# Kernel tuning notes

Hardware: AMD Instinct MI355X
Metric: run time of the kernel (lower is better)

## Reference

```python
import jax, jax.numpy as jnp
import numpy as np

N, E = 20000, 640000
D_IN, D_H, D_OUT = 128, 64, 32


def _lin_w(key, out_d, in_d):
    return jax.random.normal(key, (out_d, in_d), jnp.float32) / np.sqrt(in_d)


def setup_inputs() -> dict:
    key = jax.random.key(0)
    ks = jax.random.split(key, 16)
    x = jax.random.normal(ks[0], (N, D_IN), jnp.float32)
    edge_index = jax.random.randint(ks[1], (2, E), 0, N, jnp.int64)
    inp = {"x": x, "edge_index": edge_index}
    # SAGEConv weights: lin_l (aggregated neighbors, with bias), lin_r (root, no bias)
    inp["Wl1"] = _lin_w(ks[2], D_H, D_IN); inp["bl1"] = jnp.zeros((D_H,), jnp.float32)
    inp["Wr1"] = _lin_w(ks[3], D_H, D_IN)
    inp["Wl2"] = _lin_w(ks[4], D_H, D_H); inp["bl2"] = jnp.zeros((D_H,), jnp.float32)
    inp["Wr2"] = _lin_w(ks[5], D_H, D_H)
    inp["Wl3"] = _lin_w(ks[6], D_OUT, D_H); inp["bl3"] = jnp.zeros((D_OUT,), jnp.float32)
    inp["Wr3"] = _lin_w(ks[7], D_OUT, D_H)
    # Conv2d kernels (OIHW), all 3x3 pad 1
    inp["Wc1"] = jax.random.normal(ks[8], (D_H, 1, 3, 3), jnp.float32) / 3.0
    inp["bc1"] = jnp.zeros((D_H,), jnp.float32)
    inp["Wc2"] = jax.random.normal(ks[9], (D_H, D_H, 3, 3), jnp.float32) / np.sqrt(9 * D_H)
    inp["bc2"] = jnp.zeros((D_H,), jnp.float32)
    inp["Wc3"] = jax.random.normal(ks[10], (1, D_H, 3, 3), jnp.float32) / np.sqrt(9 * D_H)
    inp["bc3"] = jnp.zeros((1,), jnp.float32)
    # linear2 (hidden -> hidden)
    inp["W2"] = _lin_w(ks[11], D_H, D_H); inp["b2"] = jnp.zeros((D_H,), jnp.float32)
    return inp


def _sage(x, src, dst, Wl, bl, Wr):
    # PyG SAGEConv (mean aggr): lin_l(mean_{j->i} x_j) + lin_r(x_i)
    msg = x[src]  # [E, d] gather
    agg = jax.ops.segment_sum(msg, dst, num_segments=N)
    deg = jax.ops.segment_sum(jnp.ones((src.shape[0], 1), x.dtype), dst, num_segments=N)
    agg = agg / jnp.maximum(deg, 1.0)
    return agg @ Wl.T + bl + x @ Wr.T


def _conv(x, w, b):
    y = jax.lax.conv_general_dilated(x, w, (1, 1), ((1, 1), (1, 1)),
                                     dimension_numbers=("NCHW", "OIHW", "NCHW"))
    return y + b[None, :, None, None]


def reference(x, edge_index, Wl1, bl1, Wr1, Wl2, bl2, Wr2, Wl3, bl3, Wr3,
              Wc1, bc1, Wc2, bc2, Wc3, bc3, W2, b2):
    src, dst = edge_index[0], edge_index[1]
    h = _sage(x, src, dst, Wl1, bl1, Wr1)
    h = _sage(h, src, dst, Wl2, bl2, Wr2)
    h = _sage(h, src, dst, Wl2, bl2, Wr2)  # sage2 reused, as in source
    out_1 = h
    h4 = h[None, None]                     # [1,1,N,D_H]
    out = _conv(h4, Wc1, bc1)              # [1,D_H,N,D_H]
    out = _conv(out, Wc2, bc2)             # dropout is identity at inference
    out = _conv(out, Wc3, bc3)             # [1,1,N,D_H]
    out = out[0, 0] + out_1
    out = out @ W2.T + b2
    h = _sage(out, src, dst, Wl2, bl2, Wr2)
    h = _sage(h, src, dst, Wl2, bl2, Wr2)
    h = _sage(h, src, dst, Wl3, bl3, Wr3)
    return h
```

## Files before the change

kernel.cpp:

```cpp
#include <hip/hip_runtime.h>

#define NN 20000
#define NE 640000
#define NBUK 79

__device__ __forceinline__ int probe_stride(const int* __restrict__ ei32) {
  int lane = threadIdx.x & 63;
  int v = ei32[2 * lane + 1];
  unsigned long long nz = __ballot(v != 0);
  return (nz == 0ull) ? 2 : 1;
}

__global__ __launch_bounds__(256) void k_histB(const int* __restrict__ ei,
                                               int* __restrict__ bins, int E) {
  __shared__ int lb[NBUK];
  int tid = threadIdx.x;
  int st = probe_stride(ei);
  for (int i = tid; i < NBUK; i += 256) lb[i] = 0;
  __syncthreads();
  int e0 = blockIdx.x * 4096;
#pragma unroll
  for (int t = 0; t < 16; ++t) {
    int e = e0 + t * 256 + tid;
    if (e < E) atomicAdd(&lb[ei[(size_t)(E + e) * st] >> 8], 1);
  }
  __syncthreads();
  for (int i = tid; i < NBUK; i += 256)
    if (lb[i]) atomicAdd(&bins[i], lb[i]);
}

__global__ __launch_bounds__(128) void k_scan79(const int* __restrict__ bins,
                                                int* __restrict__ bbase,
                                                int* __restrict__ bcur,
                                                int* __restrict__ rowptr,
                                                int E, int N) {
  __shared__ int lds[128];
  int tid = threadIdx.x;
  int mine = (tid < NBUK) ? bins[tid] : 0;
  lds[tid] = mine;
  __syncthreads();
  for (int off = 1; off < 128; off <<= 1) {
    int v = (tid >= off) ? lds[tid - off] : 0;
    __syncthreads();
    lds[tid] += v;
    __syncthreads();
  }
  int ex = lds[tid] - mine;
  if (tid <= NBUK) {
    bbase[tid] = ex;
    if (tid < NBUK) bcur[tid] = ex;
  }
  if (tid == 0) rowptr[N] = E;
}

__global__ __launch_bounds__(256) void k_part(const int* __restrict__ ei,
                                              int* __restrict__ bcur,
                                              unsigned long long* __restrict__ ebuf,
                                              int E) {
  __shared__ int lcnt[NBUK];
  __shared__ int lbase[NBUK];
  int tid = threadIdx.x;
  int st = probe_stride(ei);
  for (int i = tid; i < NBUK; i += 256) lcnt[i] = 0;
  __syncthreads();
  int e0 = blockIdx.x * 4096;
  int srcv[16], dstv[16], lrank[16], bk[16];
  int n = 0;
#pragma unroll
  for (int t = 0; t < 16; ++t) {
    int e = e0 + t * 256 + tid;
    if (e < E) {
      int s = ei[(size_t)e * st];
      int d = ei[(size_t)(E + e) * st];
      int b = d >> 8;
      srcv[n] = s; dstv[n] = d; bk[n] = b;
      lrank[n] = atomicAdd(&lcnt[b], 1);
      ++n;
    }
  }
  __syncthreads();
  for (int i = tid; i < NBUK; i += 256)
    lbase[i] = atomicAdd(&bcur[i], lcnt[i]);
  __syncthreads();
  for (int t = 0; t < n; ++t) {
    int pos = lbase[bk[t]] + lrank[t];
    ebuf[pos] = ((unsigned long long)(unsigned)dstv[t] << 32) | (unsigned)srcv[t];
  }
}

__global__ __launch_bounds__(256) void k_sortb(
    const unsigned long long* __restrict__ ebuf, const int* __restrict__ bbase,
    int* __restrict__ rowptr, float* __restrict__ invdeg,
    int* __restrict__ csr, int N) {
  __shared__ int lcnt[256];
  __shared__ int lcur[256];
  __shared__ int wsum[4];
  int b = blockIdx.x;
  int tid = threadIdx.x;
  int base = bbase[b], n = bbase[b + 1] - base;
  lcnt[tid] = 0;
  __syncthreads();
  for (int e = tid; e < n; e += 256) {
    int d = (int)(ebuf[base + e] >> 32);
    atomicAdd(&lcnt[d - (b << 8)], 1);
  }
  __syncthreads();
  int c = lcnt[tid];
  int lane = tid & 63, wid = tid >> 6;
  int s = c;
#pragma unroll
  for (int off = 1; off < 64; off <<= 1) {
    int v = __shfl_up(s, off, 64);
    if (lane >= off) s += v;
  }
  if (lane == 63) wsum[wid] = s;
  __syncthreads();
  int woff = 0;
  for (int w = 0; w < wid; ++w) woff += wsum[w];
  int pref = woff + s - c;
  int gnode = (b << 8) + tid;
  if (gnode < N) {
    rowptr[gnode] = base + pref;
    invdeg[gnode] = 1.0f / (float)(c < 1 ? 1 : c);
  }
  lcur[tid] = pref;
  __syncthreads();
  for (int e = tid; e < n; e += 256) {
    unsigned long long pk = ebuf[base + e];
    int d = (int)(pk >> 32);
    int pos = atomicAdd(&lcur[d - (b << 8)], 1);
    csr[base + pos] = (int)(unsigned)pk;
  }
}

__device__ __forceinline__ bool maskB(int var, int o2, int o1) {
  int s = o2 + o1;
  switch (var) {
    case 0: return (o2 >= 0) && (s >= 0);
    case 1: return s >= -1;
    case 3: return s <= 1;
    case 4: return (o2 <= 0) && (s <= 0);
    default: return true;
  }
}

__global__ __launch_bounds__(256) void k_setup2(
    const float* __restrict__ Wc1, const float* __restrict__ Wc2,
    const float* __restrict__ Wc3, const float* __restrict__ bc1,
    const float* __restrict__ bc2, const float* __restrict__ bc3,
    const float* __restrict__ Wl1, const float* __restrict__ Wr1,
    const float* __restrict__ Wl2, const float* __restrict__ Wr2,
    const float* __restrict__ Wl3, const float* __restrict__ Wr3,
    const float* __restrict__ W2, const float* __restrict__ b2,
    float* __restrict__ T729, float* __restrict__ beta5,
    float* __restrict__ Wf, float* __restrict__ bf,
    float* __restrict__ Wt1, float* __restrict__ Wt2,
    float* __restrict__ Wt3, float* __restrict__ W2t) {
  int b = blockIdx.x, tid = threadIdx.x;
  if (b == 0) {
    __shared__ float W3[576];
    __shared__ float S9s[5184];
    __shared__ float W1s[576];
    for (int e = tid; e < 576; e += 256) { W3[e] = Wc3[e]; W1s[e] = Wc1[e]; }
    __syncthreads();
    for (int bb = tid; bb < 576; bb += 256) {
      float acc[9];
#pragma unroll
      for (int a = 0; a < 9; ++a) acc[a] = 0.0f;
#pragma unroll 4
      for (int o = 0; o < 64; ++o) {
        float w2 = Wc2[o * 576 + bb];
#pragma unroll
        for (int a = 0; a < 9; ++a) acc[a] += W3[o * 9 + a] * w2;
      }
#pragma unroll
      for (int a = 0; a < 9; ++a) S9s[a * 576 + bb] = acc[a];
    }
    __syncthreads();
    for (int c = tid; c < 729; c += 256) {
      int kx0  = c % 3;
      int dl1e = (c / 3) % 3;
      int dl2e = (c / 9) % 3;
      int ky0  = (c / 27) % 3;
      int ky1  = (c / 81) % 3;
      int ky2  = c / 243;
      const float* s9 = &S9s[(ky2 * 3 + dl2e) * 576 + ky1 * 3 + dl1e];
      const float* w1 = &W1s[ky0 * 3 + kx0];
      float t = 0.0f;
#pragma unroll 8
      for (int i = 0; i < 64; ++i) t += s9[i * 9] * w1[i * 9];
      T729[c] = t;
    }
  } else if (b <= 5) {
    __shared__ float S2[576];
    __shared__ float W3b[576];
    __shared__ float B2[64];
    __shared__ float part[256];
    int var = b - 1;
    for (int e = tid; e < 576; e += 256) {
      int o = e / 9, r = e - o * 9;
      float t = 0.0f;
      for (int i = 0; i < 64; ++i) t += Wc2[o * 576 + i * 9 + r] * bc1[i];
      S2[e] = t;
      W3b[e] = Wc3[e];
    }
    if (tid < 64) B2[tid] = bc2[tid];
    __syncthreads();
    int u = tid & 63, oc = tid >> 6;
    float s = 0.0f;
    for (int ky2 = 0; ky2 < 3; ++ky2) {
      int o2 = ky2 - 1;
      bool okA = (var == 0) ? (o2 >= 0) : (var == 4) ? (o2 <= 0) : true;
      if (!okA) continue;
      for (int dl2 = -1; dl2 <= 1; ++dl2) {
        int p = u + dl2; if ((unsigned)p >= 64u) continue;
        float sel[9];
#pragma unroll
        for (int ky1 = 0; ky1 < 3; ++ky1) {
          int o1 = ky1 - 1;
          bool mb = maskB(var, o2, o1);
#pragma unroll
          for (int dl1 = -1; dl1 <= 1; ++dl1) {
            int pq = p + dl1;
            sel[ky1 * 3 + dl1 + 1] = (mb && (unsigned)pq < 64u) ? 1.0f : 0.0f;
          }
        }
#pragma unroll 4
        for (int oo = 0; oo < 16; ++oo) {
          int o = oc * 16 + oo;
          float inner = B2[o];
#pragma unroll
          for (int r = 0; r < 9; ++r) inner += S2[o * 9 + r] * sel[r];
          s += W3b[o * 9 + ky2 * 3 + (dl2 + 1)] * inner;
        }
      }
    }
    part[tid] = s;
    __syncthreads();
    if (tid < 64) {
      beta5[var * 64 + tid] =
          bc3[0] + part[tid] + part[64 + tid] + part[128 + tid] + part[192 + tid];
    }
  } else if (b <= 38) {
    int gidx = (b - 6) * 256 + tid;
    if (gidx < 8192) {
      int w = gidx >> 7, u = gidx & 127;
      const float* wsrc = (u < 64) ? &Wl2[u * 64] : &Wr2[(u - 64) * 64];
      float s = 0.0f;
#pragma unroll 4
      for (int k = 0; k < 64; ++k) s += W2[k * 64 + w] * wsrc[k];
      Wf[gidx] = s;
    } else if (gidx < 8320) {
      int u = gidx - 8192;
      const float* wsrc = (u < 64) ? &Wl2[u * 64] : &Wr2[(u - 64) * 64];
      float s = 0.0f;
#pragma unroll 4
      for (int k = 0; k < 64; ++k) s += b2[k] * wsrc[k];
      bf[u] = s;
    }
  } else {
    int idx = (b - 39) * 256 + tid;
    if (idx < 16384) {
      int w = idx >> 7, u = idx & 127;
      Wt1[idx] = (u < 64) ? Wl1[u * 128 + w] : Wr1[(u - 64) * 128 + w];
    } else if (idx < 24576) {
      int t = idx - 16384;
      int w = t >> 7, u = t & 127;
      Wt2[t] = (u < 64) ? Wl2[u * 64 + w] : Wr2[(u - 64) * 64 + w];
    } else if (idx < 28672) {
      int t = idx - 24576;
      int w = t >> 6, u = t & 63;
      Wt3[t] = (u < 32) ? Wl3[u * 64 + w] : Wr3[(u - 32) * 64 + w];
    } else {
      int t = idx - 28672;
      int w = t >> 6, u = t & 63;
      W2t[t] = W2[u * 64 + w];
    }
  }
}

__global__ __launch_bounds__(256) void k_m5(const float* __restrict__ T729,
                                            float* __restrict__ M5T) {
  __shared__ float Ts[729];
  int tid = threadIdx.x;
  for (int e = tid; e < 729; e += 256) Ts[e] = T729[e];
  __syncthreads();
  int idx = blockIdx.x * 256 + tid;
  if (idx >= 15680) return;
  int jw = idx % 7;
  int u  = (idx / 7) % 64;
  int d  = (idx / 448) % 7;
  int var = idx / 3136;
  int w = u + jw - 3;
  float s = 0.0f;
  if (w >= 0 && w < 64) {
    for (int ky2 = 0; ky2 < 3; ++ky2) {
      int o2 = ky2 - 1;
      for (int ky1 = 0; ky1 < 3; ++ky1) {
        int o1 = ky1 - 1;
        if (!maskB(var, o2, o1)) continue;
        int o0 = (d - 3) - o2 - o1;
        if (o0 < -1 || o0 > 1) continue;
        int ky0 = o0 + 1;
        int cbase = ((ky2 * 3 + ky1) * 3 + ky0) * 27;
#pragma unroll
        for (int kx0 = 0; kx0 < 3; ++kx0) {
          int jq = jw - kx0;
          if ((unsigned)jq >= 5u) continue;
          int q = u + jq - 2;
          if ((unsigned)q >= 64u) continue;
#pragma unroll
          for (int dl2e = 0; dl2e < 3; ++dl2e) {
            int p = u + dl2e - 1;
            if ((unsigned)p >= 64u) continue;
            int dl1e = jq - dl2e;
            if ((unsigned)dl1e >= 3u) continue;
            s += Ts[cbase + dl2e * 9 + dl1e * 3 + kx0];
          }
        }
      }
    }
  }
  if (d == 3 && jw == 3) s += 1.0f;
  M5T[(var * 49 + d * 7 + jw) * 64 + u] = s;
}

template <int C, int K>
__global__ __launch_bounds__(256) void k_gemm(const float* __restrict__ X,
                                              const float* __restrict__ Wt,
                                              const float* __restrict__ bias,
                                              float* __restrict__ out, int N) {
  constexpr int ROWS = 16;
  constexpr int RPT = ROWS * C / 256;
  __shared__ float Xs[ROWS * K];
  int y0 = blockIdx.x * ROWS;
  {
    const float4* src = (const float4*)(X + (size_t)y0 * K);
    float4* dst = (float4*)Xs;
#pragma unroll
    for (int v = 0; v < ROWS * K / 4 / 256; ++v)
      dst[v * 256 + threadIdx.x] = src[v * 256 + threadIdx.x];
  }
  __syncthreads();
  int u = threadIdx.x % C;
  int rg = threadIdx.x / C;
  float acc[RPT];
  float bv = bias ? bias[u] : 0.0f;
#pragma unroll
  for (int k = 0; k < RPT; ++k) acc[k] = bv;
#pragma unroll 2
  for (int w0 = 0; w0 < K; w0 += 4) {
    float m0 = Wt[(w0 + 0) * C + u];
    float m1 = Wt[(w0 + 1) * C + u];
    float m2 = Wt[(w0 + 2) * C + u];
    float m3 = Wt[(w0 + 3) * C + u];
    const float* xs = &Xs[(rg * RPT) * K + w0];
#pragma unroll
    for (int k = 0; k < RPT; ++k) {
      float4 h = *(const float4*)(xs + k * K);
      acc[k] += m0 * h.x + m1 * h.y + m2 * h.z + m3 * h.w;
    }
  }
#pragma unroll
  for (int k = 0; k < RPT; ++k)
    out[(size_t)(y0 + rg * RPT + k) * C + u] = acc[k];
}

template <int C>
__global__ __launch_bounds__(256) void k_fused(const float* __restrict__ yzin,
                                               const int* __restrict__ csr,
                                               const int* __restrict__ rowptr,
                                               const float* __restrict__ invdeg,
                                               const float* __restrict__ bl,
                                               const float* __restrict__ Wt,
                                               float* __restrict__ out, int N) {
  constexpr int FV = 16;
  constexpr int G  = 4;
  constexpr int S4 = 32;
  constexpr int CAP = 64;
  __shared__ int idxs[16 * CAP];
  __shared__ float htile[16 * 64];
  int tid = threadIdx.x;
  int w = tid >> 6, lane = tid & 63;
  int base = blockIdx.x * 16;
  int beg_r[4], m_r[4], end_r[4];
#pragma unroll
  for (int rr = 0; rr < 4; ++rr) {
    int node = base + w * 4 + rr;
    int beg = rowptr[node], end = rowptr[node + 1];
    beg_r[rr] = beg; end_r[rr] = end;
    int cnt = end - beg;
    int m = cnt < CAP ? cnt : CAP;
    m_r[rr] = m;
    int* my = &idxs[(w * 4 + rr) * CAP];
    for (int k = lane; k < m; k += 64) my[k] = csr[beg + k];
  }
  __syncthreads();
  int g = lane / FV, f = lane % FV;
  const float4* yz4 = (const float4*)yzin;
#pragma unroll
  for (int rr = 0; rr < 4; ++rr) {
    int node = base + w * 4 + rr;
    const int* my = &idxs[(w * 4 + rr) * CAP];
    int m = m_r[rr];
    float a0x=0,a0y=0,a0z=0,a0w=0, a1x=0,a1y=0,a1z=0,a1w=0;
    float a2x=0,a2y=0,a2z=0,a2w=0, a3x=0,a3y=0,a3z=0,a3w=0;
    int j = g;
    for (; j + 3 * G < m; j += 4 * G) {
      int s0 = my[j], s1 = my[j + G], s2 = my[j + 2 * G], s3 = my[j + 3 * G];
      float4 v0 = yz4[(size_t)s0 * S4 + f];
      float4 v1 = yz4[(size_t)s1 * S4 + f];
      float4 v2 = yz4[(size_t)s2 * S4 + f];
      float4 v3 = yz4[(size_t)s3 * S4 + f];
      a0x += v0.x; a0y += v0.y; a0z += v0.z; a0w += v0.w;
      a1x += v1.x; a1y += v1.y; a1z += v1.z; a1w += v1.w;
      a2x += v2.x; a2y += v2.y; a2z += v2.z; a2w += v2.w;
      a3x += v3.x; a3y += v3.y; a3z += v3.z; a3w += v3.w;
    }
    for (; j < m; j += G) {
      int s0 = my[j];
      float4 v0 = yz4[(size_t)s0 * S4 + f];
      a0x += v0.x; a0y += v0.y; a0z += v0.z; a0w += v0.w;
    }
    for (int jj = beg_r[rr] + CAP + g; jj < end_r[rr]; jj += G) {
      int s0 = csr[jj];
      float4 v0 = yz4[(size_t)s0 * S4 + f];
      a0x += v0.x; a0y += v0.y; a0z += v0.z; a0w += v0.w;
    }
    float ax = (a0x + a1x) + (a2x + a3x);
    float ay = (a0y + a1y) + (a2y + a3y);
    float az = (a0z + a1z) + (a2z + a3z);
    float aw = (a0w + a1w) + (a2w + a3w);
#pragma unroll
    for (int mm = FV; mm < 64; mm <<= 1) {
      ax += __shfl_xor(ax, mm, 64);
      ay += __shfl_xor(ay, mm, 64);
      az += __shfl_xor(az, mm, 64);
      aw += __shfl_xor(aw, mm, 64);
    }
    if (g == 0) {
      float4 root = yz4[(size_t)node * S4 + FV + f];
      float4 bv = ((const float4*)bl)[f];
      float id = invdeg[node];
      float4 o;
      o.x = ax * id + bv.x + root.x;
      o.y = ay * id + bv.y + root.y;
      o.z = az * id + bv.z + root.z;
      o.w = aw * id + bv.w + root.w;
      ((float4*)htile)[(w * 4 + rr) * 16 + f] = o;
    }
  }
  __syncthreads();
  constexpr int RPT = 16 * C / 256;
  int u = tid % C, rg = tid / C;
  float acc[RPT];
#pragma unroll
  for (int k = 0; k < RPT; ++k) acc[k] = 0.0f;
#pragma unroll 2
  for (int w0 = 0; w0 < 64; w0 += 4) {
    float m0 = Wt[(w0 + 0) * C + u];
    float m1 = Wt[(w0 + 1) * C + u];
    float m2 = Wt[(w0 + 2) * C + u];
    float m3 = Wt[(w0 + 3) * C + u];
    const float* xs = &htile[(rg * RPT) * 64 + w0];
#pragma unroll
    for (int k = 0; k < RPT; ++k) {
      float4 h4 = *(const float4*)(xs + k * 64);
      acc[k] += m0 * h4.x + m1 * h4.y + m2 * h4.z + m3 * h4.w;
    }
  }
#pragma unroll
  for (int k = 0; k < RPT; ++k)
    out[(size_t)(base + rg * RPT + k) * C + u] = acc[k];
}

__global__ __launch_bounds__(256) void k_applyfused(
    const float* __restrict__ h, const float* __restrict__ M5T,
    const float* __restrict__ beta5, const float* __restrict__ Wf,
    const float* __restrict__ bf, float* __restrict__ out, int N) {
  __shared__ float hs[22 * 70];
  __shared__ float htile[16 * 64];
  int tid = threadIdx.x;
  int bstart = blockIdx.x * 16;
  for (int idx = tid; idx < 22 * 70; idx += 256) {
    int row = idx / 70, col = idx - row * 70;
    int y = bstart - 3 + row;
    int ww = col - 3;
    float v = 0.0f;
    if ((unsigned)y < (unsigned)N && (unsigned)ww < 64u)
      v = h[(size_t)y * 64 + ww];
    hs[idx] = v;
  }
  __syncthreads();
  int u = tid & 63, g = tid >> 6;
  int lr0 = g * 4;
  int gstart = bstart + lr0;
  const float* basep = &hs[lr0 * 70 + u];
  bool interior = (gstart >= 2) && (gstart + 3 <= N - 3);
  if (interior) {
    float c[49];
#pragma unroll
    for (int t = 0; t < 49; ++t) c[t] = M5T[(2 * 49 + t) * 64 + u];
    float bet = beta5[2 * 64 + u];
    float acc[4];
#pragma unroll
    for (int k = 0; k < 4; ++k) acc[k] = bet;
#pragma unroll
    for (int rr = 0; rr < 10; ++rr) {
      float t7[7];
#pragma unroll
      for (int jw = 0; jw < 7; ++jw) t7[jw] = basep[rr * 70 + jw];
#pragma unroll
      for (int d = 0; d < 7; ++d) {
        int k = rr - d;
        if (k >= 0 && k < 4) {
#pragma unroll
          for (int jw = 0; jw < 7; ++jw) acc[k] += c[d * 7 + jw] * t7[jw];
        }
      }
    }
#pragma unroll
    for (int k = 0; k < 4; ++k) htile[(lr0 + k) * 64 + u] = acc[k];
  } else {
    for (int k = 0; k < 4; ++k) {
      int y = gstart + k;
      int var = (y == 0) ? 0 : (y == 1) ? 1 : (y == N - 2) ? 3 : (y == N - 1) ? 4 : 2;
      float acc = beta5[var * 64 + u];
      for (int d = 0; d < 7; ++d)
        for (int jw = 0; jw < 7; ++jw)
          acc += M5T[(var * 49 + d * 7 + jw) * 64 + u] * basep[(k + d) * 70 + jw];
      htile[(lr0 + k) * 64 + u] = acc;
    }
  }
  __syncthreads();
  int u2 = tid % 128, rg = tid / 128;
  float acc2[8];
  float bv = bf[u2];
#pragma unroll
  for (int k = 0; k < 8; ++k) acc2[k] = bv;
#pragma unroll 2
  for (int w0 = 0; w0 < 64; w0 += 4) {
    float m0 = Wf[(w0 + 0) * 128 + u2];
    float m1 = Wf[(w0 + 1) * 128 + u2];
    float m2 = Wf[(w0 + 2) * 128 + u2];
    float m3 = Wf[(w0 + 3) * 128 + u2];
    const float* xs = &htile[(rg * 8) * 64 + w0];
#pragma unroll
    for (int k = 0; k < 8; ++k) {
      float4 h4 = *(const float4*)(xs + k * 64);
      acc2[k] += m0 * h4.x + m1 * h4.y + m2 * h4.z + m3 * h4.w;
    }
  }
#pragma unroll
  for (int k = 0; k < 8; ++k)
    out[(size_t)(bstart + rg * 8 + k) * 128 + u2] = acc2[k];
}

template <int DH>
__global__ __launch_bounds__(256) void k_agg(const float* __restrict__ yz,
                                             const int* __restrict__ csr,
                                             const int* __restrict__ rowptr,
                                             const float* __restrict__ invdeg,
                                             const float* __restrict__ bl,
                                             float* __restrict__ out, int N) {
  constexpr int FV = DH / 4;
  constexpr int G  = 64 / FV;
  constexpr int S4 = DH / 2;
  constexpr int CAP = 256;
  __shared__ int idxs[4 * CAP];
  int wid = threadIdx.x >> 6, lane = threadIdx.x & 63;
  int node = blockIdx.x * 4 + wid;
  int beg = rowptr[node], end = rowptr[node + 1];
  int cnt = end - beg;
  int m = cnt < CAP ? cnt : CAP;
  int* my = &idxs[wid * CAP];
  for (int k = lane; k < m; k += 64) my[k] = csr[beg + k];
  __syncthreads();
  int g = lane / FV, f = lane % FV;
  const float4* yz4 = (const float4*)yz;
  float a0x=0,a0y=0,a0z=0,a0w=0, a1x=0,a1y=0,a1z=0,a1w=0;
  float a2x=0,a2y=0,a2z=0,a2w=0, a3x=0,a3y=0,a3z=0,a3w=0;
  int j = g;
  for (; j + 3 * G < m; j += 4 * G) {
    int s0 = my[j], s1 = my[j + G], s2 = my[j + 2 * G], s3 = my[j + 3 * G];
    float4 v0 = yz4[(size_t)s0 * S4 + f];
    float4 v1 = yz4[(size_t)s1 * S4 + f];
    float4 v2 = yz4[(size_t)s2 * S4 + f];
    float4 v3 = yz4[(size_t)s3 * S4 + f];
    a0x += v0.x; a0y += v0.y; a0z += v0.z; a0w += v0.w;
    a1x += v1.x; a1y += v1.y; a1z += v1.z; a1w += v1.w;
    a2x += v2.x; a2y += v2.y; a2z += v2.z; a2w += v2.w;
    a3x += v3.x; a3y += v3.y; a3z += v3.z; a3w += v3.w;
  }
  for (; j < m; j += G) {
    int s0 = my[j];
    float4 v0 = yz4[(size_t)s0 * S4 + f];
    a0x += v0.x; a0y += v0.y; a0z += v0.z; a0w += v0.w;
  }
  for (int jj = beg + CAP + g; jj < end; jj += G) {
    int s0 = csr[jj];
    float4 v0 = yz4[(size_t)s0 * S4 + f];
    a0x += v0.x; a0y += v0.y; a0z += v0.z; a0w += v0.w;
  }
  float ax = (a0x + a1x) + (a2x + a3x);
  float ay = (a0y + a1y) + (a2y + a3y);
  float az = (a0z + a1z) + (a2z + a3z);
  float aw = (a0w + a1w) + (a2w + a3w);
#pragma unroll
  for (int mm = FV; mm < 64; mm <<= 1) {
    ax += __shfl_xor(ax, mm, 64);
    ay += __shfl_xor(ay, mm, 64);
    az += __shfl_xor(az, mm, 64);
    aw += __shfl_xor(aw, mm, 64);
  }
  if (g == 0) {
    float4 root = yz4[(size_t)node * S4 + FV + f];
    float4 bv = ((const float4*)bl)[f];
    float id = invdeg[node];
    float4 o;
    o.x = ax * id + bv.x + root.x;
    o.y = ay * id + bv.y + root.y;
    o.z = az * id + bv.z + root.z;
    o.w = aw * id + bv.w + root.w;
    ((float4*)out)[(size_t)node * FV + f] = o;
  }
}

extern "C" void kernel_launch(void* const* d_in, const int* in_sizes, int n_in,
                              void* d_out, int out_size, void* d_ws, size_t ws_size,
                              hipStream_t stream) {
  const int N = NN, E = NE;
  const float* x   = (const float*)d_in[0];
  const int*   ei  = (const int*)d_in[1];
  const float* Wl1 = (const float*)d_in[2];
  const float* bl1 = (const float*)d_in[3];
  const float* Wr1 = (const float*)d_in[4];
  const float* Wl2 = (const float*)d_in[5];
  const float* bl2 = (const float*)d_in[6];
  const float* Wr2 = (const float*)d_in[7];
  const float* Wl3 = (const float*)d_in[8];
  const float* bl3 = (const float*)d_in[9];
  const float* Wr3 = (const float*)d_in[10];
  const float* Wc1 = (const float*)d_in[11];
  const float* bc1 = (const float*)d_in[12];
  const float* Wc2 = (const float*)d_in[13];
  const float* bc2 = (const float*)d_in[14];
  const float* Wc3 = (const float*)d_in[15];
  const float* bc3 = (const float*)d_in[16];
  const float* W2  = (const float*)d_in[17];
  const float* b2  = (const float*)d_in[18];

  char* ws = (char*)d_ws;
  size_t off = 0;
  auto alloc = [&](size_t bytes) -> void* {
    off = (off + 255) & ~(size_t)255;
    void* p = ws + off;
    off += bytes;
    return p;
  };
  int*   rowptr = (int*)alloc((size_t)(N + 1) * 4);
  float* invdeg = (float*)alloc((size_t)N * 4);
  int*   csr    = (int*)alloc((size_t)E * 4);
  unsigned long long* ebuf = (unsigned long long*)alloc((size_t)E * 8);
  int*   bins   = (int*)alloc(128 * 4);
  int*   bbase  = (int*)alloc(128 * 4);
  int*   bcur   = (int*)alloc(128 * 4);
  float* Wt1    = (float*)alloc(128 * 128 * 4);
  float* Wt2    = (float*)alloc(64 * 128 * 4);
  float* Wt3    = (float*)alloc(64 * 64 * 4);
  float* W2t    = (float*)alloc(64 * 64 * 4);
  float* Wf     = (float*)alloc(64 * 128 * 4);
  float* bf     = (float*)alloc(128 * 4);
  float* T729   = (float*)alloc(729 * 4);
  float* M5T    = (float*)alloc(15680 * 4);
  float* beta5  = (float*)alloc(320 * 4);
  float* yzA    = (float*)alloc((size_t)N * 128 * 4);
  float* yzB    = (float*)alloc((size_t)N * 128 * 4);
  float* hA     = (float*)alloc((size_t)N * 64 * 4);
  (void)ws_size; (void)in_sizes; (void)n_in; (void)out_size;

  const int gG = N / 16;
  const int gA = N / 4;
  const int gP = (E + 4095) / 4096;

  hipMemsetAsync(bins, 0, 128 * 4, stream);
  k_histB<<<gP, 256, 0, stream>>>(ei, bins, E);
  k_scan79<<<1, 128, 0, stream>>>(bins, bbase, bcur, rowptr, E, N);
  k_part<<<gP, 256, 0, stream>>>(ei, bcur, ebuf, E);
  k_sortb<<<NBUK, 256, 0, stream>>>(ebuf, bbase, rowptr, invdeg, csr, N);

  k_setup2<<<167, 256, 0, stream>>>(Wc1, Wc2, Wc3, bc1, bc2, bc3,
                                    Wl1, Wr1, Wl2, Wr2, Wl3, Wr3, W2, b2,
                                    T729, beta5, Wf, bf, Wt1, Wt2, Wt3, W2t);
  k_m5<<<62, 256, 0, stream>>>(T729, M5T);

  k_gemm<128, 128><<<gG, 256, 0, stream>>>(x, Wt1, nullptr, yzA, N);
  k_fused<128><<<gG, 256, 0, stream>>>(yzA, csr, rowptr, invdeg, bl1, Wt2, yzB, N);
  k_fused<128><<<gG, 256, 0, stream>>>(yzB, csr, rowptr, invdeg, bl2, Wt2, yzA, N);
  k_agg<64><<<gA, 256, 0, stream>>>(yzA, csr, rowptr, invdeg, bl2, hA, N);
  k_applyfused<<<gG, 256, 0, stream>>>(hA, M5T, beta5, Wf, bf, yzB, N);
  k_fused<128><<<gG, 256, 0, stream>>>(yzB, csr, rowptr, invdeg, bl2, Wt2, yzA, N);
  k_fused<64><<<gG, 256, 0, stream>>>(yzA, csr, rowptr, invdeg, bl2, Wt3, yzB, N);
  k_agg<32><<<gA, 256, 0, stream>>>(yzB, csr, rowptr, invdeg, bl3, (float*)d_out, N);
}
```

Before: 323.3 us.

## Fold last three linear SAGE layers into 32-wide polynomial propagation

Because the last three SAGE layers are linear, their weight products are expanded algebraically into precomputed matrices (S, G, Wg). The applyfused stage then emits four 32-wide projections per node, and three 32-wide aggregations apply the mean operator Horner-style. This replaces two 128-wide fused aggregate+GEMM passes and one 32-wide aggregation with three 32-wide gathers. It adds two small setup kernels and changes floating-point summation order.

```diff
diff --git a/kernel.cpp b/kernel.cpp
--- a/kernel.cpp
+++ b/kernel.cpp
@@ -152,10 +152,12 @@
     const float* __restrict__ Wl2, const float* __restrict__ Wr2,
     const float* __restrict__ Wl3, const float* __restrict__ Wr3,
     const float* __restrict__ W2, const float* __restrict__ b2,
+    const float* __restrict__ bl2,
     float* __restrict__ T729, float* __restrict__ beta5,
     float* __restrict__ Wf, float* __restrict__ bf,
     float* __restrict__ Wt1, float* __restrict__ Wt2,
-    float* __restrict__ Wt3, float* __restrict__ W2t) {
+    float* __restrict__ Wt3, float* __restrict__ W2t,
+    float* __restrict__ Sbuf, float* __restrict__ c5) {
   int b = blockIdx.x, tid = threadIdx.x;
   if (b == 0) {
     __shared__ float W3[576];
@@ -271,11 +273,85 @@
       int t = idx - 24576;
       int w = t >> 6, u = t & 63;
       Wt3[t] = (u < 32) ? Wl3[u * 64 + w] : Wr3[(u - 32) * 64 + w];
-    } else {
+    } else if (idx < 32768) {
       int t = idx - 28672;
       int w = t >> 6, u = t & 63;
       W2t[t] = W2[u * 64 + w];
-    }
+    } else if (idx < 45056) {
+      int t2 = idx - 32768;
+      int m = t2 >> 12, e = t2 & 4095;
+      int i = e >> 6, j = e & 63;
+      float s = 0.0f;
+#pragma unroll 4
+      for (int k = 0; k < 64; ++k) {
+        float wlj = Wl2[j * 64 + k], wrj = Wr2[j * 64 + k];
+        float wli = Wl2[k * 64 + i], wri = Wr2[k * 64 + i];
+        if (m == 0) s += wli * wlj;
+        else if (m == 1) s += wri * wlj + wli * wrj;
+        else s += wri * wrj;
+      }
+      Sbuf[t2] = s;
+    } else if (idx < 45120) {
+      int j = idx - 45056;
+      float s = bl2[j];
+      for (int i = 0; i < 64; ++i)
+        s += bl2[i] * (Wl2[j * 64 + i] + Wr2[j * 64 + i]);
+      c5[j] = s;
+    }
+  }
+}
+
+__global__ __launch_bounds__(256) void k_setupG(
+    const float* __restrict__ Sbuf, const float* __restrict__ c5,
+    const float* __restrict__ Wl3, const float* __restrict__ Wr3,
+    const float* __restrict__ bl3, float* __restrict__ Gbuf,
+    float* __restrict__ c32) {
+  int b = blockIdx.x, tid = threadIdx.x;
+  if (b < 32) {
+    int idx = b * 256 + tid;
+    int kblk = idx >> 11;
+    int rem = idx & 2047;
+    int t = rem >> 5, j = rem & 31;
+    const float* S2p = Sbuf;
+    const float* S1p = Sbuf + 4096;
+    const float* S0p = Sbuf + 8192;
+    const float* pa = (kblk == 0) ? S2p : (kblk == 1) ? S1p : (kblk == 2) ? S0p : nullptr;
+    const float* pb = (kblk == 1) ? S2p : (kblk == 2) ? S1p : (kblk == 3) ? S0p : nullptr;
+    float s = 0.0f;
+#pragma unroll 4
+    for (int k = 0; k < 64; ++k) {
+      if (pa) s += pa[t * 64 + k] * Wl3[j * 64 + k];
+      if (pb) s += pb[t * 64 + k] * Wr3[j * 64 + k];
+    }
+    Gbuf[idx] = s;
+  } else if (tid < 32) {
+    float s = bl3[tid];
+    for (int k = 0; k < 64; ++k)
+      s += c5[k] * (Wl3[tid * 64 + k] + Wr3[tid * 64 + k]);
+    c32[tid] = s;
+  }
+}
+
+__global__ __launch_bounds__(256) void k_setupWg(
+    const float* __restrict__ Gbuf, const float* __restrict__ W2,
+    const float* __restrict__ b2, float* __restrict__ Wg,
+    float* __restrict__ bg) {
+  int b = blockIdx.x, tid = threadIdx.x;
+  if (b < 32) {
+    int idx = b * 256 + tid;
+    int w = idx >> 7, u = idx & 127;
+    int kblk = u >> 5, j = u & 31;
+    const float* gp = Gbuf + kblk * 2048 + j;
+    float s = 0.0f;
+#pragma unroll 4
+    for (int t = 0; t < 64; ++t) s += W2[t * 64 + w] * gp[t * 32];
+    Wg[idx] = s;
+  } else if (tid < 128) {
+    int kblk = tid >> 5, j = tid & 31;
+    const float* gp = Gbuf + kblk * 2048 + j;
+    float s = 0.0f;
+    for (int t = 0; t < 64; ++t) s += b2[t] * gp[t * 32];
+    bg[tid] = s;
   }
 }
 
@@ -476,8 +552,8 @@
 
 __global__ __launch_bounds__(256) void k_applyfused(
     const float* __restrict__ h, const float* __restrict__ M5T,
-    const float* __restrict__ beta5, const float* __restrict__ Wf,
-    const float* __restrict__ bf, float* __restrict__ out, int N) {
+    const float* __restrict__ beta5, const float* __restrict__ Wg,
+    const float* __restrict__ bg, float* __restrict__ wout, int N) {
   __shared__ float hs[22 * 70];
   __shared__ float htile[16 * 64];
   int tid = threadIdx.x;
@@ -535,15 +611,15 @@
   __syncthreads();
   int u2 = tid % 128, rg = tid / 128;
   float acc2[8];
-  float bv = bf[u2];
+  float bv = bg[u2];
 #pragma unroll
   for (int k = 0; k < 8; ++k) acc2[k] = bv;
 #pragma unroll 2
   for (int w0 = 0; w0 < 64; w0 += 4) {
-    float m0 = Wf[(w0 + 0) * 128 + u2];
-    float m1 = Wf[(w0 + 1) * 128 + u2];
-    float m2 = Wf[(w0 + 2) * 128 + u2];
-    float m3 = Wf[(w0 + 3) * 128 + u2];
+    float m0 = Wg[(w0 + 0) * 128 + u2];
+    float m1 = Wg[(w0 + 1) * 128 + u2];
+    float m2 = Wg[(w0 + 2) * 128 + u2];
+    float m3 = Wg[(w0 + 3) * 128 + u2];
     const float* xs = &htile[(rg * 8) * 64 + w0];
 #pragma unroll
     for (int k = 0; k < 8; ++k) {
@@ -551,9 +627,12 @@
       acc2[k] += m0 * h4.x + m1 * h4.y + m2 * h4.z + m3 * h4.w;
     }
   }
-#pragma unroll
-  for (int k = 0; k < 8; ++k)
-    out[(size_t)(bstart + rg * 8 + k) * 128 + u2] = acc2[k];
+  int kb = u2 >> 5, jj = u2 & 31;
+#pragma unroll
+  for (int k = 0; k < 8; ++k) {
+    int node = bstart + rg * 8 + k;
+    wout[((size_t)kb * N + node) * 32 + jj] = acc2[k];
+  }
 }
 
 template <int DH>
@@ -622,6 +701,76 @@
     o.y = ay * id + bv.y + root.y;
     o.z = az * id + bv.z + root.z;
     o.w = aw * id + bv.w + root.w;
+    ((float4*)out)[(size_t)node * FV + f] = o;
+  }
+}
+
+__global__ __launch_bounds__(256) void k_agg32(
+    const float* __restrict__ src, const int* __restrict__ csr,
+    const int* __restrict__ rowptr, const float* __restrict__ invdeg,
+    const float* __restrict__ add, const float* __restrict__ cvec,
+    float* __restrict__ out, int N) {
+  constexpr int FV = 8;
+  constexpr int G  = 8;
+  constexpr int CAP = 256;
+  __shared__ int idxs[4 * CAP];
+  int wid = threadIdx.x >> 6, lane = threadIdx.x & 63;
+  int node = blockIdx.x * 4 + wid;
+  int beg = rowptr[node], end = rowptr[node + 1];
+  int cnt = end - beg;
+  int m = cnt < CAP ? cnt : CAP;
+  int* my = &idxs[wid * CAP];
+  for (int k = lane; k < m; k += 64) my[k] = csr[beg + k];
+  __syncthreads();
+  int g = lane / FV, f = lane % FV;
+  const float4* sr4 = (const float4*)src;
+  float a0x=0,a0y=0,a0z=0,a0w=0, a1x=0,a1y=0,a1z=0,a1w=0;
+  float a2x=0,a2y=0,a2z=0,a2w=0, a3x=0,a3y=0,a3z=0,a3w=0;
+  int j = g;
+  for (; j + 3 * G < m; j += 4 * G) {
+    int s0 = my[j], s1 = my[j + G], s2 = my[j + 2 * G], s3 = my[j + 3 * G];
+    float4 v0 = sr4[(size_t)s0 * FV + f];
+    float4 v1 = sr4[(size_t)s1 * FV + f];
+    float4 v2 = sr4[(size_t)s2 * FV + f];
+    float4 v3 = sr4[(size_t)s3 * FV + f];
+    a0x += v0.x; a0y += v0.y; a0z += v0.z; a0w += v0.w;
+    a1x += v1.x; a1y += v1.y; a1z += v1.z; a1w += v1.w;
+    a2x += v2.x; a2y += v2.y; a2z += v2.z; a2w += v2.w;
+    a3x += v3.x; a3y += v3.y; a3z += v3.z; a3w += v3.w;
+  }
+  for (; j < m; j += G) {
+    int s0 = my[j];
+    float4 v0 = sr4[(size_t)s0 * FV + f];
+    a0x += v0.x; a0y += v0.y; a0z += v0.z; a0w += v0.w;
+  }
+  for (int jj = beg + CAP + g; jj < end; jj += G) {
+    int s0 = csr[jj];
+    float4 v0 = sr4[(size_t)s0 * FV + f];
+    a0x += v0.x; a0y += v0.y; a0z += v0.z; a0w += v0.w;
+  }
+  float ax = (a0x + a1x) + (a2x + a3x);
+  float ay = (a0y + a1y) + (a2y + a3y);
+  float az = (a0z + a1z) + (a2z + a3z);
+  float aw = (a0w + a1w) + (a2w + a3w);
+#pragma unroll
+  for (int mm = FV; mm < 64; mm <<= 1) {
+    ax += __shfl_xor(ax, mm, 64);
+    ay += __shfl_xor(ay, mm, 64);
+    az += __shfl_xor(az, mm, 64);
+    aw += __shfl_xor(aw, mm, 64);
+  }
+  if (g == 0) {
+    float4 av = ((const float4*)add)[(size_t)node * FV + f];
+    float id = invdeg[node];
+    float4 o;
+    o.x = ax * id + av.x;
+    o.y = ay * id + av.y;
+    o.z = az * id + av.z;
+    o.w = aw * id + av.w;
+    if (cvec != nullptr) {
+      float4 cv = ((const float4*)cvec)[f];
+      o.x += cv.x; o.y += cv.y; o.z += cv.z; o.w += cv.w;
+    }
     ((float4*)out)[(size_t)node * FV + f] = o;
   }
 }
@@ -674,9 +823,18 @@
   float* T729   = (float*)alloc(729 * 4);
   float* M5T    = (float*)alloc(15680 * 4);
   float* beta5  = (float*)alloc(320 * 4);
+  float* Sbuf   = (float*)alloc(12288 * 4);
+  float* c5     = (float*)alloc(64 * 4);
+  float* Gbuf   = (float*)alloc(8192 * 4);
+  float* Wg     = (float*)alloc(8192 * 4);
+  float* bg     = (float*)alloc(128 * 4);
+  float* c32    = (float*)alloc(32 * 4);
   float* yzA    = (float*)alloc((size_t)N * 128 * 4);
   float* yzB    = (float*)alloc((size_t)N * 128 * 4);
   float* hA     = (float*)alloc((size_t)N * 64 * 4);
+  float* wbuf   = (float*)alloc((size_t)4 * N * 32 * 4);
+  float* s1buf  = (float*)alloc((size_t)N * 32 * 4);
+  float* s2buf  = (float*)alloc((size_t)N * 32 * 4);
   (void)ws_size; (void)in_sizes; (void)n_in; (void)out_size;
 
   const int gG = N / 16;
@@ -689,17 +847,24 @@
   k_part<<<gP, 256, 0, stream>>>(ei, bcur, ebuf, E);
   k_sortb<<<NBUK, 256, 0, stream>>>(ebuf, bbase, rowptr, invdeg, csr, N);
 
-  k_setup2<<<167, 256, 0, stream>>>(Wc1, Wc2, Wc3, bc1, bc2, bc3,
-                                    Wl1, Wr1, Wl2, Wr2, Wl3, Wr3, W2, b2,
-                                    T729, beta5, Wf, bf, Wt1, Wt2, Wt3, W2t);
+  k_setup2<<<216, 256, 0, stream>>>(Wc1, Wc2, Wc3, bc1, bc2, bc3,
+                                    Wl1, Wr1, Wl2, Wr2, Wl3, Wr3, W2, b2, bl2,
+                                    T729, beta5, Wf, bf, Wt1, Wt2, Wt3, W2t,
+                                    Sbuf, c5);
+  k_setupG<<<33, 256, 0, stream>>>(Sbuf, c5, Wl3, Wr3, bl3, Gbuf, c32);
+  k_setupWg<<<33, 256, 0, stream>>>(Gbuf, W2, b2, Wg, bg);
   k_m5<<<62, 256, 0, stream>>>(T729, M5T);
 
   k_gemm<128, 128><<<gG, 256, 0, stream>>>(x, Wt1, nullptr, yzA, N);
   k_fused<128><<<gG, 256, 0, stream>>>(yzA, csr, rowptr, invdeg, bl1, Wt2, yzB, N);
   k_fused<128><<<gG, 256, 0, stream>>>(yzB, csr, rowptr, invdeg, bl2, Wt2, yzA, N);
   k_agg<64><<<gA, 256, 0, stream>>>(yzA, csr, rowptr, invdeg, bl2, hA, N);
-  k_applyfused<<<gG, 256, 0, stream>>>(hA, M5T, beta5, Wf, bf, yzB, N);
-  k_fused<128><<<gG, 256, 0, stream>>>(yzB, csr, rowptr, invdeg, bl2, Wt2, yzA, N);
-  k_fused<64><<<gG, 256, 0, stream>>>(yzA, csr, rowptr, invdeg, bl2, Wt3, yzB, N);
-  k_agg<32><<<gA, 256, 0, stream>>>(yzB, csr, rowptr, invdeg, bl3, (float*)d_out, N);
-}
+  k_applyfused<<<gG, 256, 0, stream>>>(hA, M5T, beta5, Wg, bg, wbuf, N);
+  const float* w3 = wbuf;
+  const float* w2p = wbuf + (size_t)N * 32;
+  const float* w1p = wbuf + (size_t)2 * N * 32;
+  const float* w0p = wbuf + (size_t)3 * N * 32;
+  k_agg32<<<gA, 256, 0, stream>>>(w3, csr, rowptr, invdeg, w2p, nullptr, s1buf, N);
+  k_agg32<<<gA, 256, 0, stream>>>(s1buf, csr, rowptr, invdeg, w1p, nullptr, s2buf, N);
+  k_agg32<<<gA, 256, 0, stream>>>(s2buf, csr, rowptr, invdeg, w0p, c32, (float*)d_out, N);
+}
```

After: 324.4 us. No clear change (+0.4%).
